# Performance work log

Measured on AMD Instinct MI355X. Metric: run time of the kernel, lower is better.

The kernel has to match this reference:

```python
import jax, jax.numpy as jnp
import numpy as np

N_NODES = 100000
N_EDGES = 1600000
F_IN = 128
HID = 128
N_GRAPHS = 64


def setup_inputs() -> dict:
    key = jax.random.key(0)
    ks = jax.random.split(key, 12)
    x = jax.random.normal(ks[0], (N_NODES, F_IN), dtype=jnp.float32)
    edge_index = jax.random.randint(ks[1], (2, N_EDGES), 0, N_NODES, dtype=jnp.int32)
    batch = jnp.sort(jax.random.randint(ks[2], (N_NODES,), 0, N_GRAPHS, dtype=jnp.int32))
    s = 1.0 / np.sqrt(F_IN)
    W1 = jax.random.normal(ks[3], (F_IN, HID), dtype=jnp.float32) * s
    b1 = jnp.zeros((HID,), jnp.float32)
    W2 = jax.random.normal(ks[4], (HID, HID), dtype=jnp.float32) * s
    b2 = jnp.zeros((HID,), jnp.float32)
    W3 = jax.random.normal(ks[5], (HID, HID), dtype=jnp.float32) * s
    b3 = jnp.zeros((HID,), jnp.float32)
    Wc1 = jax.random.normal(ks[6], (HID, HID // 2), dtype=jnp.float32) * s
    bc1 = jnp.zeros((HID // 2,), jnp.float32)
    Wc2 = jax.random.normal(ks[7], (HID // 2, 1), dtype=jnp.float32) * (1.0 / np.sqrt(HID // 2))
    bc2 = jnp.zeros((1,), jnp.float32)
    return {"x": x, "edge_index": edge_index, "batch": batch,
            "W1": W1, "b1": b1, "W2": W2, "b2": b2, "W3": W3, "b3": b3,
            "Wc1": Wc1, "bc1": bc1, "Wc2": Wc2, "bc2": bc2}


def _gcn_conv(x, W, b, src, dst, norm, n_nodes):
    # PyG GCNConv: x' = D^-1/2 (A+I) D^-1/2 (x W) + b  (self-loops already in src/dst)
    h = x @ W                                   # [N, H] small GEMM
    msg = h[src] * norm[:, None]                # [E+N, H] gather (memory bound)
    out = jax.ops.segment_sum(msg, dst, num_segments=n_nodes)  # scatter-add
    return out + b


def reference(x, edge_index, batch, W1, b1, W2, b2, W3, b3, Wc1, bc1, Wc2, bc2):
    n = x.shape[0]
    loop = jnp.arange(n, dtype=edge_index.dtype)
    src = jnp.concatenate([edge_index[0], loop])
    dst = jnp.concatenate([edge_index[1], loop])
    deg = jax.ops.segment_sum(jnp.ones_like(dst, dtype=x.dtype), dst, num_segments=n)
    dinv = jax.lax.rsqrt(jnp.maximum(deg, 1.0))
    norm = dinv[src] * dinv[dst]                # [E+N]

    h = jax.nn.elu(_gcn_conv(x, W1, b1, src, dst, norm, n))   # dropout is identity in eval
    h = jax.nn.elu(_gcn_conv(h, W2, b2, src, dst, norm, n))
    h = jax.nn.elu(_gcn_conv(h, W3, b3, src, dst, norm, n))

    # global mean pool over graphs
    sums = jax.ops.segment_sum(h, batch, num_segments=N_GRAPHS)
    cnts = jax.ops.segment_sum(jnp.ones((n,), h.dtype), batch, num_segments=N_GRAPHS)
    g = sums / jnp.maximum(cnts, 1.0)[:, None]  # [G, H]

    z = jax.nn.relu(g @ Wc1 + bc1)
    logits = z @ Wc2 + bc2
    return jax.nn.sigmoid(logits)               # [G, 1]
```

## Files before the change

### kernel.cpp

```cpp
#include <hip/hip_runtime.h>
#include <cstdint>
#include <cstddef>


#define SUBCAP 512
#define CSRCAP 4608
#define TILE 4096

typedef __attribute__((ext_vector_type(8))) short short8;
typedef __attribute__((ext_vector_type(4))) float f32x4;
typedef __attribute__((ext_vector_type(2))) _Float16 h16x2;

__device__ __forceinline__ float bf2f(uint32_t u) {
  return __uint_as_float(u << 16);
}
__device__ __forceinline__ uint32_t f2bf(float f) {
  uint32_t x = __float_as_uint(f);
  return (x + 0x7FFFu + ((x >> 16) & 1u)) >> 16;
}

union H16 { _Float16 h; uint16_t u; };
union H2U { h16x2 h; uint32_t u; };

__device__ __forceinline__ uint32_t f2e5m2(float f) {
  f = fminf(fmaxf(f, -30000.f), 30000.f);
  H16 cv;
  cv.h = (_Float16)f;
  uint32_t h = cv.u;
  uint32_t r = h + 0x7Fu + ((h >> 8) & 1u);
  return (r >> 8) & 0xFFu;
}

__device__ __forceinline__ float e5m2f(uint32_t b) {
  H16 cv;
  cv.u = (uint16_t)(b << 8);
  return (float)cv.h;
}


__global__ __launch_bounds__(256) void bucket_scatter(const int* __restrict__ src,
                                                      const int* __restrict__ dst,
                                                      int* __restrict__ bcur,
                                                      uint32_t* __restrict__ ebuf,
                                                      int nE, int nbuk) {
  uint32_t xcc;
  asm("s_getreg_b32 %0, hwreg(HW_REG_XCC_ID)" : "=s"(xcc));
  __shared__ int lhist[1024];
  __shared__ int gbase[1024];
  int t = threadIdx.x;
  for (int i = t; i < nbuk; i += 256) lhist[i] = 0;
  __syncthreads();

  int e0 = blockIdx.x * TILE;
  int myd[16], mys[16], myrank[16];
#pragma unroll
  for (int j = 0; j < 16; ++j) {
    int e = e0 + t + j * 256;
    if (e < nE) {
      int d = dst[e];
      myd[j] = d;
      mys[j] = src[e];
      myrank[j] = atomicAdd(&lhist[d >> 7], 1);
    } else {
      myd[j] = -1;
    }
  }
  __syncthreads();
  for (int i = t; i < nbuk; i += 256) {
    int c = lhist[i];
    gbase[i] = c ? atomicAdd(&bcur[((i << 3) | (int)xcc) * 16], c) : 0;
  }
  __syncthreads();
#pragma unroll
  for (int j = 0; j < 16; ++j) {
    if (myd[j] >= 0) {
      int b = myd[j] >> 7;
      int pos = gbase[b] + myrank[j];
      if (pos < SUBCAP) {
        int sub = (b << 3) | (int)xcc;
        ebuf[(size_t)sub * SUBCAP + pos] =
            ((uint32_t)(myd[j] & 127) << 20) | (uint32_t)mys[j];
      }
    }
  }
}

__global__ __launch_bounds__(256) void bucket_build(const uint32_t* __restrict__ ebuf,
                                                    const int* __restrict__ bcur,
                                                    int* __restrict__ deg,
                                                    float* __restrict__ dinv,
                                                    int* __restrict__ offs,
                                                    int* __restrict__ csr, int n) {
  int b = blockIdx.x;
  int base = b << 7;
  __shared__ int hist[128];
  __shared__ int pre[128];
  __shared__ int lcur[128];
  int t = threadIdx.x;
  if (t < 128) hist[t] = 0;
  __syncthreads();
  int cnts[8];
#pragma unroll
  for (int x = 0; x < 8; ++x) {
    int sub = (b << 3) | x;
    int cnt = min(bcur[sub * 16], SUBCAP);
    cnts[x] = cnt;
    const uint32_t* eb = ebuf + (size_t)sub * SUBCAP;
    for (int e = t; e < cnt; e += 256) atomicAdd(&hist[eb[e] >> 20], 1);
  }
  __syncthreads();
  if (t < 128) pre[t] = (hist[t] + 3) & ~3;
  __syncthreads();
  for (int d = 1; d < 128; d <<= 1) {
    int v = (t >= d && t < 128) ? pre[t - d] : 0;
    __syncthreads();
    if (t < 128) pre[t] += v;
    __syncthreads();
  }
  if (t < 128) {
    int dg = hist[t];
    int start = b * CSRCAP + pre[t] - ((dg + 3) & ~3);
    lcur[t] = start;
    if (base + t < n) {
      deg[base + t] = dg;
      dinv[base + t] = rsqrtf((float)(dg + 1));
      offs[base + t] = start;
    }
  }
  __syncthreads();
#pragma unroll
  for (int x = 0; x < 8; ++x) {
    int sub = (b << 3) | x;
    int cnt = cnts[x];
    const uint32_t* eb = ebuf + (size_t)sub * SUBCAP;
    for (int e = t; e < cnt; e += 256) {
      uint32_t ed = eb[e];
      int pos = atomicAdd(&lcur[ed >> 20], 1);
      csr[pos] = (int)((ed & 0xFFFFFu) << 7);
    }
  }
}


__global__ __launch_bounds__(256) void cvt_wt(const float* __restrict__ W1,
                                              const float* __restrict__ W2,
                                              const float* __restrict__ W3,
                                              uint16_t* __restrict__ WT) {
  int id = blockIdx.x * 256 + threadIdx.x;
  if (id >= 3 * 16384) return;
  int w = id >> 14;
  int rem = id & 16383;
  int k = rem >> 7, nn = rem & 127;
  const float* W = (w == 0) ? W1 : ((w == 1) ? W2 : W3);
  WT[w * 16384 + nn * 128 + k] = (uint16_t)f2bf(W[k * 128 + nn]);
}


template <bool F32IN>
__global__ __launch_bounds__(256) void gemm_mfma(const uint16_t* __restrict__ Xb,
                                                 const float* __restrict__ X32,
                                                 const uint16_t* __restrict__ WTb,
                                                 const float* __restrict__ dinv,
                                                 uint8_t* __restrict__ tab, int n) {
  __shared__ uint16_t sW[128 * 136];
  int t = threadIdx.x;
#pragma unroll
  for (int i = 0; i < 8; ++i) {
    int j = t + i * 256;
    int r = j >> 4, c = j & 15;
    float4 v = ((const float4*)WTb)[j];
    *(float4*)(sW + r * 136 + c * 8) = v;
  }
  __syncthreads();

  int wave = t >> 6, lane = t & 63;
  int quad = lane >> 4, l15 = lane & 15;
  int m = blockIdx.x * 64 + wave * 16 + l15;
  int mm = min(m, n - 1);

  short8 a[4];
#pragma unroll
  for (int kc = 0; kc < 4; ++kc) {
    if constexpr (F32IN) {
      const float* p = X32 + (size_t)mm * 128 + kc * 32 + quad * 8;
      float4 lo = *(const float4*)p;
      float4 hi = *(const float4*)(p + 4);
      a[kc] = (short8){(short)f2bf(lo.x), (short)f2bf(lo.y),
                       (short)f2bf(lo.z), (short)f2bf(lo.w),
                       (short)f2bf(hi.x), (short)f2bf(hi.y),
                       (short)f2bf(hi.z), (short)f2bf(hi.w)};
    } else {
      a[kc] = *(const short8*)(Xb + (size_t)mm * 128 + kc * 32 + quad * 8);
    }
  }

  f32x4 acc[8];
#pragma unroll
  for (int nn = 0; nn < 8; ++nn) acc[nn] = (f32x4){0.f, 0.f, 0.f, 0.f};

#pragma unroll
  for (int nn = 0; nn < 8; ++nn) {
    int nrow = nn * 16 + l15;
#pragma unroll
    for (int kc = 0; kc < 4; ++kc) {
      short8 b = *(const short8*)(sW + nrow * 136 + kc * 32 + quad * 8);
      acc[nn] = __builtin_amdgcn_mfma_f32_16x16x32_bf16(a[kc], b, acc[nn], 0, 0, 0);
    }
  }

  int mrow = blockIdx.x * 64 + wave * 16 + quad * 4;
#pragma unroll
  for (int r = 0; r < 4; ++r) {
    int row = mrow + r;
    if (row < n) {
      float dn = dinv[row];
#pragma unroll
      for (int nn = 0; nn < 8; ++nn) {
        tab[(size_t)row * 128 + nn * 16 + l15] = (uint8_t)f2e5m2(acc[nn][r] * dn);
      }
    }
  }
}


__device__ __forceinline__ void acc_pk(uint32_t u, h16x2& a01, h16x2& a23) {
  H2U p01, p23;
  p01.u = __builtin_amdgcn_perm(u, 0u, 0x05010400u);
  p23.u = __builtin_amdgcn_perm(u, 0u, 0x07010600u);
  a01 += p01.h;
  a23 += p23.h;
}

__global__ __launch_bounds__(256) void gather_fused(const uint8_t* __restrict__ tab,
                                                    const int* __restrict__ csr,
                                                    const int* __restrict__ offs,
                                                    const int* __restrict__ deg,
                                                    const float* __restrict__ dinv,
                                                    const float* __restrict__ b,
                                                    uint16_t* __restrict__ out, int n) {
  int node = blockIdx.x * 8 + (threadIdx.x >> 5);
  if (node >= n) return;
  int l = threadIdx.x & 31;
  int c = l * 4;
  const uint8_t* tabc = tab + c;
  int e0 = offs[node];
  int e1 = e0 + deg[node];
  h16x2 a01 = (h16x2){(_Float16)0.f, (_Float16)0.f};
  h16x2 a23 = (h16x2){(_Float16)0.f, (_Float16)0.f};

  int e = e0;
  for (; e + 7 < e1; e += 8) {
    int4 ca = *(const int4*)(csr + e);
    int4 cb = *(const int4*)(csr + e + 4);
    uint32_t u[8];
    u[0] = *(const uint32_t*)(tabc + ca.x);
    u[1] = *(const uint32_t*)(tabc + ca.y);
    u[2] = *(const uint32_t*)(tabc + ca.z);
    u[3] = *(const uint32_t*)(tabc + ca.w);
    u[4] = *(const uint32_t*)(tabc + cb.x);
    u[5] = *(const uint32_t*)(tabc + cb.y);
    u[6] = *(const uint32_t*)(tabc + cb.z);
    u[7] = *(const uint32_t*)(tabc + cb.w);
#pragma unroll
    for (int j = 0; j < 8; ++j) acc_pk(u[j], a01, a23);
  }
  if (e + 3 < e1) {
    int4 ca = *(const int4*)(csr + e);
    uint32_t u[4];
    u[0] = *(const uint32_t*)(tabc + ca.x);
    u[1] = *(const uint32_t*)(tabc + ca.y);
    u[2] = *(const uint32_t*)(tabc + ca.z);
    u[3] = *(const uint32_t*)(tabc + ca.w);
#pragma unroll
    for (int j = 0; j < 4; ++j) acc_pk(u[j], a01, a23);
    e += 4;
  }
  for (; e < e1; ++e) acc_pk(*(const uint32_t*)(tabc + csr[e]), a01, a23);

  float a0 = (float)a01.x, a1 = (float)a01.y;
  float a2 = (float)a23.x, a3 = (float)a23.y;

  float dn = dinv[node];
  uint32_t uh = *(const uint32_t*)(tabc + node * 128);
  float4 bb = *(const float4*)(b + c);
  float o0 = (a0 + e5m2f(uh & 0xFFu)) * dn + bb.x;
  float o1 = (a1 + e5m2f((uh >> 8) & 0xFFu)) * dn + bb.y;
  float o2 = (a2 + e5m2f((uh >> 16) & 0xFFu)) * dn + bb.z;
  float o3 = (a3 + e5m2f(uh >> 24)) * dn + bb.w;
  o0 = o0 > 0.f ? o0 : expm1f(o0);
  o1 = o1 > 0.f ? o1 : expm1f(o1);
  o2 = o2 > 0.f ? o2 : expm1f(o2);
  o3 = o3 > 0.f ? o3 : expm1f(o3);
  uint2 po;
  po.x = f2bf(o0) | (f2bf(o1) << 16);
  po.y = f2bf(o2) | (f2bf(o3) << 16);
  *(uint2*)(out + (size_t)node * 128 + c) = po;
}


__global__ __launch_bounds__(64) void cnt_bs_kernel(const int* __restrict__ batch,
                                                    int* __restrict__ cnt, int n) {
  int g = threadIdx.x;
  auto lb = [&](int v) {
    int lo = 0, hi = n;
    while (lo < hi) {
      int mid = (lo + hi) >> 1;
      if (batch[mid] < v) lo = mid + 1; else hi = mid;
    }
    return lo;
  };
  int a = lb(g);
  int bnd = lb(g + 1);
  cnt[g] = bnd - a;
}

__global__ __launch_bounds__(128) void pool_kernel(const uint16_t* __restrict__ h,
                                                   const int* __restrict__ batch,
                                                   float* __restrict__ pool, int n) {
  int f = threadIdx.x;
  int i0 = blockIdx.x * 64;
  int iend = min(i0 + 64, n);
  __shared__ int sb[64];
  if (threadIdx.x < 64 && i0 + threadIdx.x < n) sb[threadIdx.x] = batch[i0 + threadIdx.x];
  __syncthreads();
  float acc = 0.f;
  int cur = sb[0];
  for (int i = i0; i < iend; ++i) {
    int g = sb[i - i0];
    if (g != cur) {
      atomicAdd(&pool[cur * 128 + f], acc);
      acc = 0.f;
      cur = g;
    }
    acc += bf2f((uint32_t)h[(size_t)i * 128 + f]);
  }
  atomicAdd(&pool[cur * 128 + f], acc);
}

__global__ __launch_bounds__(256) void classifier_kernel(const float* __restrict__ pool,
                                                         const int* __restrict__ cnt,
                                                         const float* __restrict__ Wc1,
                                                         const float* __restrict__ bc1,
                                                         const float* __restrict__ Wc2,
                                                         const float* __restrict__ bc2,
                                                         float* __restrict__ out) {
  __shared__ float g[64 * 128];
  __shared__ float z[64 * 64];
  int t = threadIdx.x;
  for (int i = t; i < 64 * 128; i += 256) {
    int gi = i >> 7;
    float c = (float)max(cnt[gi], 1);
    g[i] = pool[i] / c;
  }
  __syncthreads();
  for (int i = t; i < 64 * 64; i += 256) {
    int gi = i >> 6, j = i & 63;
    float acc = bc1[j];
    for (int k = 0; k < 128; ++k) acc += g[gi * 128 + k] * Wc1[k * 64 + j];
    z[i] = fmaxf(acc, 0.f);
  }
  __syncthreads();
  if (t < 64) {
    float acc = bc2[0];
    for (int j = 0; j < 64; ++j) acc += z[t * 64 + j] * Wc2[j];
    out[t] = 1.f / (1.f + expf(-acc));
  }
}

extern "C" void kernel_launch(void* const* d_in, const int* in_sizes, int n_in,
                              void* d_out, int out_size, void* d_ws, size_t ws_size,
                              hipStream_t stream) {
  const float* x   = (const float*)d_in[0];
  const int* ei    = (const int*)d_in[1];
  const int* batch = (const int*)d_in[2];
  const float* W1  = (const float*)d_in[3];
  const float* b1  = (const float*)d_in[4];
  const float* W2  = (const float*)d_in[5];
  const float* b2  = (const float*)d_in[6];
  const float* W3  = (const float*)d_in[7];
  const float* b3  = (const float*)d_in[8];
  const float* Wc1 = (const float*)d_in[9];
  const float* bc1 = (const float*)d_in[10];
  const float* Wc2 = (const float*)d_in[11];
  const float* bc2 = (const float*)d_in[12];

  int n  = in_sizes[2];
  int nE = in_sizes[1] / 2;
  const int* src = ei;
  const int* dst = ei + nE;
  int nbuk = (n + 127) >> 7;

  uint8_t*  tab  = (uint8_t*)d_ws;
  uint16_t* bufO = (uint16_t*)(tab + (size_t)n * 128);
  float* dinv    = (float*)(bufO + (size_t)n * 128);
  int*   deg     = (int*)(dinv + n);
  int*   offs    = deg + n;
  int*   bcur    = offs + n + 4;
  int*   csr     = bcur + nbuk * 8 * 16;
  uint32_t* ebuf = (uint32_t*)(csr + (size_t)nbuk * CSRCAP);
  uint16_t* WT   = (uint16_t*)(ebuf + (size_t)nbuk * 8 * SUBCAP);
  float* pool    = (float*)(WT + 3 * 16384);
  int*   cnt     = (int*)(pool + 64 * 128);
  float* out     = (float*)d_out;

  hipMemsetAsync(bcur, 0, (size_t)nbuk * 8 * 16 * sizeof(int), stream);
  bucket_scatter<<<(nE + TILE - 1) / TILE, 256, 0, stream>>>(src, dst, bcur, ebuf, nE, nbuk);
  bucket_build<<<nbuk, 256, 0, stream>>>(ebuf, bcur, deg, dinv, offs, csr, n);

  cvt_wt<<<(3 * 16384 + 255) / 256, 256, 0, stream>>>(W1, W2, W3, WT);

  const float* bs[3] = {b1, b2, b3};
  for (int l = 0; l < 3; ++l) {
    if (l == 0)
      gemm_mfma<true><<<(n + 63) / 64, 256, 0, stream>>>(nullptr, x, WT, dinv, tab, n);
    else
      gemm_mfma<false><<<(n + 63) / 64, 256, 0, stream>>>(bufO, nullptr, WT + l * 16384, dinv, tab, n);
    gather_fused<<<(n + 7) / 8, 256, 0, stream>>>(tab, csr, offs, deg, dinv, bs[l], bufO, n);
  }

  hipMemsetAsync(pool, 0, 64 * 128 * sizeof(float), stream);
  cnt_bs_kernel<<<1, 64, 0, stream>>>(batch, cnt, n);
  pool_kernel<<<(n + 63) / 64, 128, 0, stream>>>(bufO, batch, pool, n);
  classifier_kernel<<<1, 256, 0, stream>>>(pool, cnt, Wc1, bc1, Wc2, bc2, out);
}
```

Baseline: 369.2 us.

## Fuse all stages into one cooperative persistent kernel with grid syncs

Replaces the sequence of about twelve kernel launches (bucket scatter, CSR build, weight conversion, three GEMM+gather layers, pooling, classifier) with one cooperative persistent kernel. Stages are separated by grid.sync() and loop over work with grid-stride indexing, with the grid sized from occupancy queries. The aim is to remove launch gaps and per-kernel ramp-up/tail overhead. The cost is a grid-wide barrier per stage, lower occupancy than the separate launches allowed, one shared-memory size for every stage, and the weight tile being reloaded into LDS for every GEMM tile.

```diff
diff --git a/kernel.cpp b/kernel.cpp
--- a/kernel.cpp
+++ b/kernel.cpp
@@ -1,6 +1,9 @@
 #include <hip/hip_runtime.h>
+#include <hip/hip_cooperative_groups.h>
 #include <cstdint>
 #include <cstddef>
+
+namespace cg = cooperative_groups;
 
 
 #define SUBCAP 512
@@ -37,192 +40,6 @@
   return (float)cv.h;
 }
 
-
-__global__ __launch_bounds__(256) void bucket_scatter(const int* __restrict__ src,
-                                                      const int* __restrict__ dst,
-                                                      int* __restrict__ bcur,
-                                                      uint32_t* __restrict__ ebuf,
-                                                      int nE, int nbuk) {
-  uint32_t xcc;
-  asm("s_getreg_b32 %0, hwreg(HW_REG_XCC_ID)" : "=s"(xcc));
-  __shared__ int lhist[1024];
-  __shared__ int gbase[1024];
-  int t = threadIdx.x;
-  for (int i = t; i < nbuk; i += 256) lhist[i] = 0;
-  __syncthreads();
-
-  int e0 = blockIdx.x * TILE;
-  int myd[16], mys[16], myrank[16];
-#pragma unroll
-  for (int j = 0; j < 16; ++j) {
-    int e = e0 + t + j * 256;
-    if (e < nE) {
-      int d = dst[e];
-      myd[j] = d;
-      mys[j] = src[e];
-      myrank[j] = atomicAdd(&lhist[d >> 7], 1);
-    } else {
-      myd[j] = -1;
-    }
-  }
-  __syncthreads();
-  for (int i = t; i < nbuk; i += 256) {
-    int c = lhist[i];
-    gbase[i] = c ? atomicAdd(&bcur[((i << 3) | (int)xcc) * 16], c) : 0;
-  }
-  __syncthreads();
-#pragma unroll
-  for (int j = 0; j < 16; ++j) {
-    if (myd[j] >= 0) {
-      int b = myd[j] >> 7;
-      int pos = gbase[b] + myrank[j];
-      if (pos < SUBCAP) {
-        int sub = (b << 3) | (int)xcc;
-        ebuf[(size_t)sub * SUBCAP + pos] =
-            ((uint32_t)(myd[j] & 127) << 20) | (uint32_t)mys[j];
-      }
-    }
-  }
-}
-
-__global__ __launch_bounds__(256) void bucket_build(const uint32_t* __restrict__ ebuf,
-                                                    const int* __restrict__ bcur,
-                                                    int* __restrict__ deg,
-                                                    float* __restrict__ dinv,
-                                                    int* __restrict__ offs,
-                                                    int* __restrict__ csr, int n) {
-  int b = blockIdx.x;
-  int base = b << 7;
-  __shared__ int hist[128];
-  __shared__ int pre[128];
-  __shared__ int lcur[128];
-  int t = threadIdx.x;
-  if (t < 128) hist[t] = 0;
-  __syncthreads();
-  int cnts[8];
-#pragma unroll
-  for (int x = 0; x < 8; ++x) {
-    int sub = (b << 3) | x;
-    int cnt = min(bcur[sub * 16], SUBCAP);
-    cnts[x] = cnt;
-    const uint32_t* eb = ebuf + (size_t)sub * SUBCAP;
-    for (int e = t; e < cnt; e += 256) atomicAdd(&hist[eb[e] >> 20], 1);
-  }
-  __syncthreads();
-  if (t < 128) pre[t] = (hist[t] + 3) & ~3;
-  __syncthreads();
-  for (int d = 1; d < 128; d <<= 1) {
-    int v = (t >= d && t < 128) ? pre[t - d] : 0;
-    __syncthreads();
-    if (t < 128) pre[t] += v;
-    __syncthreads();
-  }
-  if (t < 128) {
-    int dg = hist[t];
-    int start = b * CSRCAP + pre[t] - ((dg + 3) & ~3);
-    lcur[t] = start;
-    if (base + t < n) {
-      deg[base + t] = dg;
-      dinv[base + t] = rsqrtf((float)(dg + 1));
-      offs[base + t] = start;
-    }
-  }
-  __syncthreads();
-#pragma unroll
-  for (int x = 0; x < 8; ++x) {
-    int sub = (b << 3) | x;
-    int cnt = cnts[x];
-    const uint32_t* eb = ebuf + (size_t)sub * SUBCAP;
-    for (int e = t; e < cnt; e += 256) {
-      uint32_t ed = eb[e];
-      int pos = atomicAdd(&lcur[ed >> 20], 1);
-      csr[pos] = (int)((ed & 0xFFFFFu) << 7);
-    }
-  }
-}
-
-
-__global__ __launch_bounds__(256) void cvt_wt(const float* __restrict__ W1,
-                                              const float* __restrict__ W2,
-                                              const float* __restrict__ W3,
-                                              uint16_t* __restrict__ WT) {
-  int id = blockIdx.x * 256 + threadIdx.x;
-  if (id >= 3 * 16384) return;
-  int w = id >> 14;
-  int rem = id & 16383;
-  int k = rem >> 7, nn = rem & 127;
-  const float* W = (w == 0) ? W1 : ((w == 1) ? W2 : W3);
-  WT[w * 16384 + nn * 128 + k] = (uint16_t)f2bf(W[k * 128 + nn]);
-}
-
-
-template <bool F32IN>
-__global__ __launch_bounds__(256) void gemm_mfma(const uint16_t* __restrict__ Xb,
-                                                 const float* __restrict__ X32,
-                                                 const uint16_t* __restrict__ WTb,
-                                                 const float* __restrict__ dinv,
-                                                 uint8_t* __restrict__ tab, int n) {
-  __shared__ uint16_t sW[128 * 136];
-  int t = threadIdx.x;
-#pragma unroll
-  for (int i = 0; i < 8; ++i) {
-    int j = t + i * 256;
-    int r = j >> 4, c = j & 15;
-    float4 v = ((const float4*)WTb)[j];
-    *(float4*)(sW + r * 136 + c * 8) = v;
-  }
-  __syncthreads();
-
-  int wave = t >> 6, lane = t & 63;
-  int quad = lane >> 4, l15 = lane & 15;
-  int m = blockIdx.x * 64 + wave * 16 + l15;
-  int mm = min(m, n - 1);
-
-  short8 a[4];
-#pragma unroll
-  for (int kc = 0; kc < 4; ++kc) {
-    if constexpr (F32IN) {
-      const float* p = X32 + (size_t)mm * 128 + kc * 32 + quad * 8;
-      float4 lo = *(const float4*)p;
-      float4 hi = *(const float4*)(p + 4);
-      a[kc] = (short8){(short)f2bf(lo.x), (short)f2bf(lo.y),
-                       (short)f2bf(lo.z), (short)f2bf(lo.w),
-                       (short)f2bf(hi.x), (short)f2bf(hi.y),
-                       (short)f2bf(hi.z), (short)f2bf(hi.w)};
-    } else {
-      a[kc] = *(const short8*)(Xb + (size_t)mm * 128 + kc * 32 + quad * 8);
-    }
-  }
-
-  f32x4 acc[8];
-#pragma unroll
-  for (int nn = 0; nn < 8; ++nn) acc[nn] = (f32x4){0.f, 0.f, 0.f, 0.f};
-
-#pragma unroll
-  for (int nn = 0; nn < 8; ++nn) {
-    int nrow = nn * 16 + l15;
-#pragma unroll
-    for (int kc = 0; kc < 4; ++kc) {
-      short8 b = *(const short8*)(sW + nrow * 136 + kc * 32 + quad * 8);
-      acc[nn] = __builtin_amdgcn_mfma_f32_16x16x32_bf16(a[kc], b, acc[nn], 0, 0, 0);
-    }
-  }
-
-  int mrow = blockIdx.x * 64 + wave * 16 + quad * 4;
-#pragma unroll
-  for (int r = 0; r < 4; ++r) {
-    int row = mrow + r;
-    if (row < n) {
-      float dn = dinv[row];
-#pragma unroll
-      for (int nn = 0; nn < 8; ++nn) {
-        tab[(size_t)row * 128 + nn * 16 + l15] = (uint8_t)f2e5m2(acc[nn][r] * dn);
-      }
-    }
-  }
-}
-
-
 __device__ __forceinline__ void acc_pk(uint32_t u, h16x2& a01, h16x2& a23) {
   H2U p01, p23;
   p01.u = __builtin_amdgcn_perm(u, 0u, 0x05010400u);
@@ -231,139 +48,324 @@
   a23 += p23.h;
 }
 
-__global__ __launch_bounds__(256) void gather_fused(const uint8_t* __restrict__ tab,
-                                                    const int* __restrict__ csr,
-                                                    const int* __restrict__ offs,
-                                                    const int* __restrict__ deg,
-                                                    const float* __restrict__ dinv,
-                                                    const float* __restrict__ b,
-                                                    uint16_t* __restrict__ out, int n) {
-  int node = blockIdx.x * 8 + (threadIdx.x >> 5);
-  if (node >= n) return;
-  int l = threadIdx.x & 31;
-  int c = l * 4;
-  const uint8_t* tabc = tab + c;
-  int e0 = offs[node];
-  int e1 = e0 + deg[node];
-  h16x2 a01 = (h16x2){(_Float16)0.f, (_Float16)0.f};
-  h16x2 a23 = (h16x2){(_Float16)0.f, (_Float16)0.f};
-
-  int e = e0;
-  for (; e + 7 < e1; e += 8) {
-    int4 ca = *(const int4*)(csr + e);
-    int4 cb = *(const int4*)(csr + e + 4);
-    uint32_t u[8];
-    u[0] = *(const uint32_t*)(tabc + ca.x);
-    u[1] = *(const uint32_t*)(tabc + ca.y);
-    u[2] = *(const uint32_t*)(tabc + ca.z);
-    u[3] = *(const uint32_t*)(tabc + ca.w);
-    u[4] = *(const uint32_t*)(tabc + cb.x);
-    u[5] = *(const uint32_t*)(tabc + cb.y);
-    u[6] = *(const uint32_t*)(tabc + cb.z);
-    u[7] = *(const uint32_t*)(tabc + cb.w);
-#pragma unroll
-    for (int j = 0; j < 8; ++j) acc_pk(u[j], a01, a23);
+__global__ __launch_bounds__(256, 4) void mega(
+    const float* __restrict__ x, const int* __restrict__ src,
+    const int* __restrict__ dst,
+    const float* __restrict__ W1, const float* __restrict__ W2,
+    const float* __restrict__ W3,
+    const float* __restrict__ b1, const float* __restrict__ b2,
+    const float* __restrict__ b3,
+    const float* __restrict__ Wc1, const float* __restrict__ bc1,
+    const float* __restrict__ Wc2, const float* __restrict__ bc2,
+    const int* __restrict__ batch,
+    int* __restrict__ bcur, uint32_t* __restrict__ ebuf,
+    int* __restrict__ deg, float* __restrict__ dinv,
+    int* __restrict__ offs, int* __restrict__ csr,
+    uint16_t* __restrict__ WT, uint8_t* __restrict__ tab,
+    uint16_t* __restrict__ bufO, float* __restrict__ pool,
+    float* __restrict__ outp,
+    int n, int nE, int nbuk) {
+  cg::grid_group grid = cg::this_grid();
+  __shared__ __align__(16) uint8_t smem[128 * 136 * 2];
+  int t = threadIdx.x;
+  int bid = blockIdx.x, G = gridDim.x;
+
+  {
+    uint32_t xcc;
+    asm("s_getreg_b32 %0, hwreg(HW_REG_XCC_ID)" : "=s"(xcc));
+    int* lhist = (int*)smem;
+    int* gbase = lhist + 1024;
+    int ntile = (nE + TILE - 1) / TILE;
+    for (int tile = bid; tile < ntile; tile += G) {
+      for (int i = t; i < nbuk; i += 256) lhist[i] = 0;
+      __syncthreads();
+      int e0 = tile * TILE;
+      int myd[16], mys[16], myrank[16];
+#pragma unroll
+      for (int j = 0; j < 16; ++j) {
+        int e = e0 + t + j * 256;
+        if (e < nE) {
+          int d = dst[e];
+          myd[j] = d;
+          mys[j] = src[e];
+          myrank[j] = atomicAdd(&lhist[d >> 7], 1);
+        } else {
+          myd[j] = -1;
+        }
+      }
+      __syncthreads();
+      for (int i = t; i < nbuk; i += 256) {
+        int c = lhist[i];
+        gbase[i] = c ? atomicAdd(&bcur[((i << 3) | (int)xcc) * 16], c) : 0;
+      }
+      __syncthreads();
+#pragma unroll
+      for (int j = 0; j < 16; ++j) {
+        if (myd[j] >= 0) {
+          int b = myd[j] >> 7;
+          int pos = gbase[b] + myrank[j];
+          if (pos < SUBCAP) {
+            int sub = (b << 3) | (int)xcc;
+            ebuf[(size_t)sub * SUBCAP + pos] =
+                ((uint32_t)(myd[j] & 127) << 20) | (uint32_t)mys[j];
+          }
+        }
+      }
+      __syncthreads();
+    }
+    for (int id = bid * 256 + t; id < 3 * 16384; id += G * 256) {
+      int w = id >> 14;
+      int rem = id & 16383;
+      int k = rem >> 7, nn = rem & 127;
+      const float* W = (w == 0) ? W1 : ((w == 1) ? W2 : W3);
+      WT[w * 16384 + nn * 128 + k] = (uint16_t)f2bf(W[k * 128 + nn]);
+    }
+    for (int id = bid * 256 + t; id < 64 * 128; id += G * 256) pool[id] = 0.f;
   }
-  if (e + 3 < e1) {
-    int4 ca = *(const int4*)(csr + e);
-    uint32_t u[4];
-    u[0] = *(const uint32_t*)(tabc + ca.x);
-    u[1] = *(const uint32_t*)(tabc + ca.y);
-    u[2] = *(const uint32_t*)(tabc + ca.z);
-    u[3] = *(const uint32_t*)(tabc + ca.w);
-#pragma unroll
-    for (int j = 0; j < 4; ++j) acc_pk(u[j], a01, a23);
-    e += 4;
+  grid.sync();
+
+  {
+    int* hist = (int*)smem;
+    int* pre = hist + 128;
+    int* lcur = pre + 128;
+    for (int b = bid; b < nbuk; b += G) {
+      int base = b << 7;
+      if (t < 128) hist[t] = 0;
+      __syncthreads();
+      int cnts[8];
+#pragma unroll
+      for (int x2 = 0; x2 < 8; ++x2) {
+        int sub = (b << 3) | x2;
+        int cnt = min(bcur[sub * 16], SUBCAP);
+        cnts[x2] = cnt;
+        const uint32_t* eb = ebuf + (size_t)sub * SUBCAP;
+        for (int e = t; e < cnt; e += 256) atomicAdd(&hist[eb[e] >> 20], 1);
+      }
+      __syncthreads();
+      if (t < 128) pre[t] = (hist[t] + 3) & ~3;
+      __syncthreads();
+      for (int d = 1; d < 128; d <<= 1) {
+        int v = (t >= d && t < 128) ? pre[t - d] : 0;
+        __syncthreads();
+        if (t < 128) pre[t] += v;
+        __syncthreads();
+      }
+      if (t < 128) {
+        int dg = hist[t];
+        int start = b * CSRCAP + pre[t] - ((dg + 3) & ~3);
+        lcur[t] = start;
+        if (base + t < n) {
+          deg[base + t] = dg;
+          dinv[base + t] = rsqrtf((float)(dg + 1));
+          offs[base + t] = start;
+        }
+      }
+      __syncthreads();
+#pragma unroll
+      for (int x2 = 0; x2 < 8; ++x2) {
+        int sub = (b << 3) | x2;
+        int cnt = cnts[x2];
+        const uint32_t* eb = ebuf + (size_t)sub * SUBCAP;
+        for (int e = t; e < cnt; e += 256) {
+          uint32_t ed = eb[e];
+          int pos = atomicAdd(&lcur[ed >> 20], 1);
+          csr[pos] = (int)((ed & 0xFFFFFu) << 7);
+        }
+      }
+      __syncthreads();
+    }
   }
-  for (; e < e1; ++e) acc_pk(*(const uint32_t*)(tabc + csr[e]), a01, a23);
-
-  float a0 = (float)a01.x, a1 = (float)a01.y;
-  float a2 = (float)a23.x, a3 = (float)a23.y;
-
-  float dn = dinv[node];
-  uint32_t uh = *(const uint32_t*)(tabc + node * 128);
-  float4 bb = *(const float4*)(b + c);
-  float o0 = (a0 + e5m2f(uh & 0xFFu)) * dn + bb.x;
-  float o1 = (a1 + e5m2f((uh >> 8) & 0xFFu)) * dn + bb.y;
-  float o2 = (a2 + e5m2f((uh >> 16) & 0xFFu)) * dn + bb.z;
-  float o3 = (a3 + e5m2f(uh >> 24)) * dn + bb.w;
-  o0 = o0 > 0.f ? o0 : expm1f(o0);
-  o1 = o1 > 0.f ? o1 : expm1f(o1);
-  o2 = o2 > 0.f ? o2 : expm1f(o2);
-  o3 = o3 > 0.f ? o3 : expm1f(o3);
-  uint2 po;
-  po.x = f2bf(o0) | (f2bf(o1) << 16);
-  po.y = f2bf(o2) | (f2bf(o3) << 16);
-  *(uint2*)(out + (size_t)node * 128 + c) = po;
-}
-
-
-__global__ __launch_bounds__(64) void cnt_bs_kernel(const int* __restrict__ batch,
-                                                    int* __restrict__ cnt, int n) {
-  int g = threadIdx.x;
-  auto lb = [&](int v) {
-    int lo = 0, hi = n;
-    while (lo < hi) {
-      int mid = (lo + hi) >> 1;
-      if (batch[mid] < v) lo = mid + 1; else hi = mid;
-    }
-    return lo;
-  };
-  int a = lb(g);
-  int bnd = lb(g + 1);
-  cnt[g] = bnd - a;
-}
-
-__global__ __launch_bounds__(128) void pool_kernel(const uint16_t* __restrict__ h,
-                                                   const int* __restrict__ batch,
-                                                   float* __restrict__ pool, int n) {
-  int f = threadIdx.x;
-  int i0 = blockIdx.x * 64;
-  int iend = min(i0 + 64, n);
-  __shared__ int sb[64];
-  if (threadIdx.x < 64 && i0 + threadIdx.x < n) sb[threadIdx.x] = batch[i0 + threadIdx.x];
-  __syncthreads();
-  float acc = 0.f;
-  int cur = sb[0];
-  for (int i = i0; i < iend; ++i) {
-    int g = sb[i - i0];
-    if (g != cur) {
-      atomicAdd(&pool[cur * 128 + f], acc);
-      acc = 0.f;
-      cur = g;
-    }
-    acc += bf2f((uint32_t)h[(size_t)i * 128 + f]);
+  grid.sync();
+
+  uint16_t* sW = (uint16_t*)smem;
+  int ntiles = (n + 63) / 64;
+  int nchunk = (n + 7) / 8;
+  const float* bs0[3] = {b1, b2, b3};
+  for (int l = 0; l < 3; ++l) {
+    const uint16_t* WTb = WT + l * 16384;
+    for (int tile = bid; tile < ntiles; tile += G) {
+      __syncthreads();
+#pragma unroll
+      for (int i = 0; i < 8; ++i) {
+        int j = t + i * 256;
+        int r = j >> 4, c = j & 15;
+        float4 v = ((const float4*)WTb)[j];
+        *(float4*)(sW + r * 136 + c * 8) = v;
+      }
+      __syncthreads();
+      int wave = t >> 6, lane = t & 63;
+      int quad = lane >> 4, l15 = lane & 15;
+      int m = tile * 64 + wave * 16 + l15;
+      int mm = min(m, n - 1);
+      short8 a[4];
+#pragma unroll
+      for (int kc = 0; kc < 4; ++kc) {
+        if (l == 0) {
+          const float* p = x + (size_t)mm * 128 + kc * 32 + quad * 8;
+          float4 lo = *(const float4*)p;
+          float4 hi = *(const float4*)(p + 4);
+          a[kc] = (short8){(short)f2bf(lo.x), (short)f2bf(lo.y),
+                           (short)f2bf(lo.z), (short)f2bf(lo.w),
+                           (short)f2bf(hi.x), (short)f2bf(hi.y),
+                           (short)f2bf(hi.z), (short)f2bf(hi.w)};
+        } else {
+          a[kc] = *(const short8*)(bufO + (size_t)mm * 128 + kc * 32 + quad * 8);
+        }
+      }
+      f32x4 acc[8];
+#pragma unroll
+      for (int nn = 0; nn < 8; ++nn) acc[nn] = (f32x4){0.f, 0.f, 0.f, 0.f};
+#pragma unroll
+      for (int nn = 0; nn < 8; ++nn) {
+        int nrow = nn * 16 + l15;
+#pragma unroll
+        for (int kc = 0; kc < 4; ++kc) {
+          short8 bfr = *(const short8*)(sW + nrow * 136 + kc * 32 + quad * 8);
+          acc[nn] = __builtin_amdgcn_mfma_f32_16x16x32_bf16(a[kc], bfr, acc[nn], 0, 0, 0);
+        }
+      }
+      int mrow = tile * 64 + wave * 16 + quad * 4;
+#pragma unroll
+      for (int r = 0; r < 4; ++r) {
+        int row = mrow + r;
+        if (row < n) {
+          float dn = dinv[row];
+#pragma unroll
+          for (int nn = 0; nn < 8; ++nn) {
+            tab[(size_t)row * 128 + nn * 16 + l15] = (uint8_t)f2e5m2(acc[nn][r] * dn);
+          }
+        }
+      }
+    }
+    grid.sync();
+    const float* bvec = bs0[l];
+    for (int chunk = bid; chunk < nchunk; chunk += G) {
+      int node = chunk * 8 + (t >> 5);
+      if (node < n) {
+        int l2 = t & 31;
+        int c = l2 * 4;
+        const uint8_t* tabc = tab + c;
+        int e0 = offs[node];
+        int e1 = e0 + deg[node];
+        h16x2 a01 = (h16x2){(_Float16)0.f, (_Float16)0.f};
+        h16x2 a23 = (h16x2){(_Float16)0.f, (_Float16)0.f};
+        int e = e0;
+        for (; e + 7 < e1; e += 8) {
+          int4 ca = *(const int4*)(csr + e);
+          int4 cb = *(const int4*)(csr + e + 4);
+          uint32_t u[8];
+          u[0] = *(const uint32_t*)(tabc + ca.x);
+          u[1] = *(const uint32_t*)(tabc + ca.y);
+          u[2] = *(const uint32_t*)(tabc + ca.z);
+          u[3] = *(const uint32_t*)(tabc + ca.w);
+          u[4] = *(const uint32_t*)(tabc + cb.x);
+          u[5] = *(const uint32_t*)(tabc + cb.y);
+          u[6] = *(const uint32_t*)(tabc + cb.z);
+          u[7] = *(const uint32_t*)(tabc + cb.w);
+#pragma unroll
+          for (int j = 0; j < 8; ++j) acc_pk(u[j], a01, a23);
+        }
+        if (e + 3 < e1) {
+          int4 ca = *(const int4*)(csr + e);
+          uint32_t u[4];
+          u[0] = *(const uint32_t*)(tabc + ca.x);
+          u[1] = *(const uint32_t*)(tabc + ca.y);
+          u[2] = *(const uint32_t*)(tabc + ca.z);
+          u[3] = *(const uint32_t*)(tabc + ca.w);
+#pragma unroll
+          for (int j = 0; j < 4; ++j) acc_pk(u[j], a01, a23);
+          e += 4;
+        }
+        for (; e < e1; ++e) acc_pk(*(const uint32_t*)(tabc + csr[e]), a01, a23);
+
+        float a0 = (float)a01.x, a1 = (float)a01.y;
+        float a2 = (float)a23.x, a3 = (float)a23.y;
+        float dn = dinv[node];
+        uint32_t uh = *(const uint32_t*)(tabc + node * 128);
+        float4 bb = *(const float4*)(bvec + c);
+        float o0 = (a0 + e5m2f(uh & 0xFFu)) * dn + bb.x;
+        float o1 = (a1 + e5m2f((uh >> 8) & 0xFFu)) * dn + bb.y;
+        float o2 = (a2 + e5m2f((uh >> 16) & 0xFFu)) * dn + bb.z;
+        float o3 = (a3 + e5m2f(uh >> 24)) * dn + bb.w;
+        o0 = o0 > 0.f ? o0 : expm1f(o0);
+        o1 = o1 > 0.f ? o1 : expm1f(o1);
+        o2 = o2 > 0.f ? o2 : expm1f(o2);
+        o3 = o3 > 0.f ? o3 : expm1f(o3);
+        uint2 po;
+        po.x = f2bf(o0) | (f2bf(o1) << 16);
+        po.y = f2bf(o2) | (f2bf(o3) << 16);
+        *(uint2*)(bufO + (size_t)node * 128 + c) = po;
+      }
+    }
+    grid.sync();
   }
-  atomicAdd(&pool[cur * 128 + f], acc);
-}
-
-__global__ __launch_bounds__(256) void classifier_kernel(const float* __restrict__ pool,
-                                                         const int* __restrict__ cnt,
-                                                         const float* __restrict__ Wc1,
-                                                         const float* __restrict__ bc1,
-                                                         const float* __restrict__ Wc2,
-                                                         const float* __restrict__ bc2,
-                                                         float* __restrict__ out) {
-  __shared__ float g[64 * 128];
-  __shared__ float z[64 * 64];
-  int t = threadIdx.x;
-  for (int i = t; i < 64 * 128; i += 256) {
-    int gi = i >> 7;
-    float c = (float)max(cnt[gi], 1);
-    g[i] = pool[i] / c;
+
+  {
+    int* sb = (int*)smem;
+    int tsub = t & 127, grp = t >> 7;
+    int npc = (n + 127) / 128;
+    for (int c = bid; c < npc; c += G) {
+      __syncthreads();
+      int i0 = c * 128 + grp * 64;
+      if (tsub < 64) {
+        int ii = c * 128 + grp * 64 + tsub;
+        sb[grp * 64 + tsub] = (ii < n) ? batch[ii] : -1;
+      }
+      __syncthreads();
+      if (i0 < n) {
+        int iend = min(i0 + 64, n);
+        float acc = 0.f;
+        int cur = sb[grp * 64];
+        for (int i = i0; i < iend; ++i) {
+          int g2 = sb[grp * 64 + (i - i0)];
+          if (g2 != cur) {
+            atomicAdd(&pool[cur * 128 + tsub], acc);
+            acc = 0.f;
+            cur = g2;
+          }
+          acc += bf2f((uint32_t)bufO[(size_t)i * 128 + tsub]);
+        }
+        atomicAdd(&pool[cur * 128 + tsub], acc);
+      }
+    }
   }
-  __syncthreads();
-  for (int i = t; i < 64 * 64; i += 256) {
-    int gi = i >> 6, j = i & 63;
-    float acc = bc1[j];
-    for (int k = 0; k < 128; ++k) acc += g[gi * 128 + k] * Wc1[k * 64 + j];
-    z[i] = fmaxf(acc, 0.f);
-  }
-  __syncthreads();
-  if (t < 64) {
-    float acc = bc2[0];
-    for (int j = 0; j < 64; ++j) acc += z[t * 64 + j] * Wc2[j];
-    out[t] = 1.f / (1.f + expf(-acc));
+  grid.sync();
+
+  if (bid == 0) {
+    uint16_t* sg = (uint16_t*)smem;
+    float* sz = (float*)(smem + 16384);
+    int* scnt = (int*)(smem + 32768);
+    if (t < 64) {
+      auto lbf = [&](int v) {
+        int lo = 0, hi = n;
+        while (lo < hi) {
+          int mid = (lo + hi) >> 1;
+          if (batch[mid] < v) lo = mid + 1; else hi = mid;
+        }
+        return lo;
+      };
+      scnt[t] = lbf(t + 1) - lbf(t);
+    }
+    __syncthreads();
+    for (int i = t; i < 64 * 128; i += 256) {
+      int gi = i >> 7;
+      float c = (float)max(scnt[gi], 1);
+      sg[i] = (uint16_t)f2bf(pool[i] / c);
+    }
+    __syncthreads();
+    for (int i = t; i < 64 * 64; i += 256) {
+      int gi = i >> 6, j = i & 63;
+      float acc = bc1[j];
+      for (int k = 0; k < 128; ++k)
+        acc += bf2f((uint32_t)sg[gi * 128 + k]) * Wc1[k * 64 + j];
+      sz[i] = fmaxf(acc, 0.f);
+    }
+    __syncthreads();
+    if (t < 64) {
+      float acc = bc2[0];
+      for (int j = 0; j < 64; ++j) acc += sz[t * 64 + j] * Wc2[j];
+      outp[t] = 1.f / (1.f + expf(-acc));
+    }
   }
 }
 
@@ -400,26 +402,24 @@
   uint32_t* ebuf = (uint32_t*)(csr + (size_t)nbuk * CSRCAP);
   uint16_t* WT   = (uint16_t*)(ebuf + (size_t)nbuk * 8 * SUBCAP);
   float* pool    = (float*)(WT + 3 * 16384);
-  int*   cnt     = (int*)(pool + 64 * 128);
-  float* out     = (float*)d_out;
+  float* outp    = (float*)d_out;
 
   hipMemsetAsync(bcur, 0, (size_t)nbuk * 8 * 16 * sizeof(int), stream);
-  bucket_scatter<<<(nE + TILE - 1) / TILE, 256, 0, stream>>>(src, dst, bcur, ebuf, nE, nbuk);
-  bucket_build<<<nbuk, 256, 0, stream>>>(ebuf, bcur, deg, dinv, offs, csr, n);
-
-  cvt_wt<<<(3 * 16384 + 255) / 256, 256, 0, stream>>>(W1, W2, W3, WT);
-
-  const float* bs[3] = {b1, b2, b3};
-  for (int l = 0; l < 3; ++l) {
-    if (l == 0)
-      gemm_mfma<true><<<(n + 63) / 64, 256, 0, stream>>>(nullptr, x, WT, dinv, tab, n);
-    else
-      gemm_mfma<false><<<(n + 63) / 64, 256, 0, stream>>>(bufO, nullptr, WT + l * 16384, dinv, tab, n);
-    gather_fused<<<(n + 7) / 8, 256, 0, stream>>>(tab, csr, offs, deg, dinv, bs[l], bufO, n);
-  }
-
-  hipMemsetAsync(pool, 0, 64 * 128 * sizeof(float), stream);
-  cnt_bs_kernel<<<1, 64, 0, stream>>>(batch, cnt, n);
-  pool_kernel<<<(n + 63) / 64, 128, 0, stream>>>(bufO, batch, pool, n);
-  classifier_kernel<<<1, 256, 0, stream>>>(pool, cnt, Wc1, bc1, Wc2, bc2, out);
-}
+
+  int bpc = 0;
+  hipOccupancyMaxActiveBlocksPerMultiprocessor(&bpc, (const void*)mega, 256, 0);
+  if (bpc < 1) bpc = 1;
+  int G = bpc * 256;
+
+  void* args[] = {
+      (void*)&x, (void*)&src, (void*)&dst,
+      (void*)&W1, (void*)&W2, (void*)&W3,
+      (void*)&b1, (void*)&b2, (void*)&b3,
+      (void*)&Wc1, (void*)&bc1, (void*)&Wc2, (void*)&bc2,
+      (void*)&batch,
+      (void*)&bcur, (void*)&ebuf, (void*)&deg, (void*)&dinv,
+      (void*)&offs, (void*)&csr,
+      (void*)&WT, (void*)&tab, (void*)&bufO, (void*)&pool, (void*)&outp,
+      (void*)&n, (void*)&nE, (void*)&nbuk};
+  hipLaunchCooperativeKernel((const void*)mega, dim3(G), dim3(256), args, 0, stream);
+}
```

After: 1.160 ms. 214% more time.
